# Kernel optimization log

Measured on AMD Instinct MI355X. Metric: run time of the kernel, lower is better.

Reference implementation:

```python
import jax, jax.numpy as jnp
import numpy as np

EPS = 1e-5
NUM_HEADS = 16


def rms_norm(x, w):
    v = jnp.mean(x * x, axis=-1, keepdims=True)
    return x * jax.lax.rsqrt(v + EPS) * w


def rotate_half_interleaved(x):
    # pairs (x0,x1) -> (-x1, x0), interleaved layout
    x1 = x[..., 0::2]
    x2 = x[..., 1::2]
    return jnp.stack([-x2, x1], axis=-1).reshape(x.shape)


def setup_inputs() -> dict:
    key = jax.random.key(0)
    ks = jax.random.split(key, 6)
    B, N, C = 2, 2048, 2048
    D = C // NUM_HEADS
    s = 1.0 / np.sqrt(C)
    return {
        "x": jax.random.normal(ks[0], (B, N, C), jnp.float32),
        "w_qkv": jax.random.normal(ks[1], (3 * C, C), jnp.float32) * s,
        "q_norm_w": jnp.ones((C,), jnp.float32),
        "k_norm_w": jnp.ones((C,), jnp.float32),
        "cos": jnp.cos(jax.random.normal(ks[2], (N, D), jnp.float32)),
        "sin": jnp.sin(jax.random.normal(ks[3], (N, D), jnp.float32)),
        "w_proj": jax.random.normal(ks[4], (C, C), jnp.float32) * s,
        "b_proj": jnp.zeros((C,), jnp.float32),
    }


def reference(x, w_qkv, q_norm_w, k_norm_w, cos, sin, w_proj, b_proj):
    B, N, C = x.shape
    H = NUM_HEADS
    D = C // H
    scale = D ** -0.5

    qkv = jnp.einsum("bnc,fc->bnf", x, w_qkv).reshape(B, N, 3, C)
    q, k, v = qkv[:, :, 0], qkv[:, :, 1], qkv[:, :, 2]

    # RMSNorm over full channel dim C (as in the torch module), then head split
    q = rms_norm(q, q_norm_w).reshape(B, N, H, D)
    k = rms_norm(k, k_norm_w).reshape(B, N, H, D)
    v = v.reshape(B, N, H, D)

    # rotary embedding (head_first=False layout [B,N,H,D])
    c = cos[None, :, None, :]
    s = sin[None, :, None, :]
    q = q * c + rotate_half_interleaved(q) * s
    k = k * c + rotate_half_interleaved(k) * s

    attn = jnp.einsum("bnhd,bmhd->bhnm", q, k) * scale  # [B,H,N,N]
    attn = jax.nn.softmax(attn, axis=-1)
    out = jnp.einsum("bhnm,bmhd->bnhd", attn, v).reshape(B, N, C)
    return jnp.einsum("bnc,oc->bno", out, w_proj) + b_proj
```

## Files before the change

kernel.cpp:

```cpp
#include <hip/hip_runtime.h>
#include <stdint.h>

typedef unsigned short u16;
typedef unsigned int   u32;
typedef _Float16 f16_t;
typedef f16_t f16x8 __attribute__((ext_vector_type(8)));
typedef float  f32x4  __attribute__((ext_vector_type(4)));

#define BB 2
#define NN 2048
#define CC 2048
#define HH 16
#define DD 128
#define FF 6144
#define MM 4096

__device__ __forceinline__ u16 f2h(float f){
    f16_t h = (f16_t)f;
    return __builtin_bit_cast(u16, h);
}
__device__ __forceinline__ float h2f(u16 b){
    return (float)__builtin_bit_cast(f16_t, b);
}
__device__ __forceinline__ f32x4 MFMA(f16x8 a, f16x8 b, f32x4 c){
    return __builtin_amdgcn_mfma_f32_16x16x32_f16(a, b, c, 0, 0, 0);
}
__device__ __forceinline__ void gld16(const void* g, void* l){
    __builtin_amdgcn_global_load_lds(
        (const __attribute__((address_space(1))) void*)(g),
        (__attribute__((address_space(3))) void*)(l), 16, 0, 0);
}
#define SB0() __builtin_amdgcn_sched_barrier(0)

__global__ void k_f2h(const float* __restrict__ a, u16* __restrict__ o, int n4){
    int i = blockIdx.x * blockDim.x + threadIdx.x;
    int stride = gridDim.x * blockDim.x;
    for (; i < n4; i += stride){
        float4 v = ((const float4*)a)[i];
        ushort4 r; r.x = f2h(v.x); r.y = f2h(v.y); r.z = f2h(v.z); r.w = f2h(v.w);
        ((ushort4*)o)[i] = r;
    }
}

template<int OUTH>
__global__ __launch_bounds__(256) void k_gemm_bt(
    const u16* __restrict__ A, const u16* __restrict__ Bw,
    float* __restrict__ outf, u16* __restrict__ outb,
    const float* __restrict__ bias, int M, int N, int K)
{
    __shared__ u16 As[3][128 * 32];
    __shared__ u16 Bs[3][128 * 32];
    const int tid  = threadIdx.x;
    const int brow = blockIdx.y * 128;
    const int bcol = blockIdx.x * 128;
    const int w = tid >> 6, lane = tid & 63;
    const int wr = w >> 1, wc = w & 1;
    const int l15 = lane & 15, g = lane >> 4;
    const int sr  = tid >> 2;
    const int scz = ((tid & 3) ^ ((tid >> 3) & 3)) * 8;
    const int gx  = (g ^ ((l15 >> 1) & 3)) * 8;

    f32x4 acc[4][4];
    #pragma unroll
    for (int i = 0; i < 4; i++)
        #pragma unroll
        for (int j = 0; j < 4; j++){
            f32x4 z = {0.f, 0.f, 0.f, 0.f};
            acc[i][j] = z;
        }

    auto stage = [&](int buf, int k0){
        gld16(&Bw[(size_t)(bcol + sr) * K + k0 + scz],      &Bs[buf][w * 512]);
        gld16(&Bw[(size_t)(bcol + sr + 64) * K + k0 + scz], &Bs[buf][2048 + w * 512]);
        gld16(&A [(size_t)(brow + sr) * K + k0 + scz],      &As[buf][w * 512]);
        gld16(&A [(size_t)(brow + sr + 64) * K + k0 + scz], &As[buf][2048 + w * 512]);
    };

    stage(0, 0);
    stage(1, 32);
    int c = 0;
    for (int k0 = 0; k0 < K; k0 += 32){
        SB0();
        __builtin_amdgcn_s_barrier();
        SB0();
        int ct = c + 2; if (ct >= 3) ct -= 3;
        if (k0 + 64 < K){
            stage(ct, k0 + 64);
            asm volatile("s_waitcnt vmcnt(8)" ::: "memory");
        } else if (k0 + 32 < K){
            asm volatile("s_waitcnt vmcnt(4)" ::: "memory");
        } else {
            asm volatile("s_waitcnt vmcnt(0)" ::: "memory");
        }
        SB0();
        __builtin_amdgcn_s_barrier();
        SB0();
        f16x8 fb[4];
        #pragma unroll
        for (int j = 0; j < 4; j++){
            int row = wc * 64 + j * 16 + l15;
            fb[j] = *(const f16x8*)&Bs[c][row * 32 + gx];
        }
        #pragma unroll
        for (int i = 0; i < 4; i++){
            int row = wr * 64 + i * 16 + l15;
            f16x8 fa = *(const f16x8*)&As[c][row * 32 + gx];
            #pragma unroll
            for (int j = 0; j < 4; j++) acc[i][j] = MFMA(fa, fb[j], acc[i][j]);
        }
        c = (c + 1 == 3) ? 0 : c + 1;
    }

    #pragma unroll
    for (int i = 0; i < 4; i++){
        #pragma unroll
        for (int j = 0; j < 4; j++){
            int colg = bcol + wc * 64 + j * 16 + l15;
            #pragma unroll
            for (int r = 0; r < 4; r++){
                int rowg = brow + wr * 64 + i * 16 + 4 * g + r;
                float v = acc[i][j][r];
                if (OUTH) outb[(size_t)rowg * N + colg] = f2h(v);
                else      outf[(size_t)rowg * N + colg] = v + bias[colg];
            }
        }
    }
}

__global__ __launch_bounds__(256) void k_norm_rope(
    const u16* __restrict__ qkv, const float* __restrict__ qw, const float* __restrict__ kw,
    const float* __restrict__ cosb, const float* __restrict__ sinb,
    u16* __restrict__ qout, u16* __restrict__ kout)
{
    const int m = blockIdx.x;
    const int b = m >> 11;
    const int n = m & 2047;
    const int t = threadIdx.x;
    const size_t base = (size_t)m * FF;
    const int e0 = t * 8;
    const float SCL = 0.08838834764831845f * 1.4426950408889634f;

    float qv[8], kvv[8];
    uint4 qa = *(const uint4*)&qkv[base + e0];
    uint4 ka = *(const uint4*)&qkv[base + CC + e0];
    {
        u32 aa[4] = {qa.x, qa.y, qa.z, qa.w};
        u32 bb[4] = {ka.x, ka.y, ka.z, ka.w};
        #pragma unroll
        for (int i = 0; i < 4; i++){
            qv[2*i]   = h2f((u16)(aa[i] & 0xffff));
            qv[2*i+1] = h2f((u16)(aa[i] >> 16));
            kvv[2*i]   = h2f((u16)(bb[i] & 0xffff));
            kvv[2*i+1] = h2f((u16)(bb[i] >> 16));
        }
    }
    float sq = 0.f, sk = 0.f;
    #pragma unroll
    for (int i = 0; i < 8; i++){ sq += qv[i]*qv[i]; sk += kvv[i]*kvv[i]; }
    #pragma unroll
    for (int o = 32; o > 0; o >>= 1){ sq += __shfl_xor(sq, o); sk += __shfl_xor(sk, o); }
    __shared__ float red[8];
    if ((t & 63) == 0){ red[(t >> 6)*2] = sq; red[(t >> 6)*2 + 1] = sk; }
    __syncthreads();
    sq = red[0] + red[2] + red[4] + red[6];
    sk = red[1] + red[3] + red[5] + red[7];
    const float rq = rsqrtf(sq * (1.f / 2048.f) + 1e-5f);
    const float rk = rsqrtf(sk * (1.f / 2048.f) + 1e-5f);

    const int h  = t >> 4;
    const int d0 = (t & 15) * 8;
    const float* cp = cosb + (size_t)n * DD + d0;
    const float* sp = sinb + (size_t)n * DD + d0;
    float qo[8], ko[8];
    #pragma unroll
    for (int j = 0; j < 8; j += 2){
        float c0 = cp[j], c1 = cp[j+1], s0 = sp[j], s1 = sp[j+1];
        float x0 = qv[j]   * rq * qw[e0 + j];
        float x1 = qv[j+1] * rq * qw[e0 + j + 1];
        qo[j]   = (x0 * c0 - x1 * s0) * SCL;
        qo[j+1] = (x1 * c1 + x0 * s1) * SCL;
        float y0 = kvv[j]   * rk * kw[e0 + j];
        float y1 = kvv[j+1] * rk * kw[e0 + j + 1];
        ko[j]   = y0 * c0 - y1 * s0;
        ko[j+1] = y1 * c1 + y0 * s1;
    }
    const size_t obase = ((size_t)(b * HH + h) * NN + n) * DD + d0;
    uint4 pq, pk;
    pq.x = (u32)f2h(qo[0]) | ((u32)f2h(qo[1]) << 16);
    pq.y = (u32)f2h(qo[2]) | ((u32)f2h(qo[3]) << 16);
    pq.z = (u32)f2h(qo[4]) | ((u32)f2h(qo[5]) << 16);
    pq.w = (u32)f2h(qo[6]) | ((u32)f2h(qo[7]) << 16);
    pk.x = (u32)f2h(ko[0]) | ((u32)f2h(ko[1]) << 16);
    pk.y = (u32)f2h(ko[2]) | ((u32)f2h(ko[3]) << 16);
    pk.z = (u32)f2h(ko[4]) | ((u32)f2h(ko[5]) << 16);
    pk.w = (u32)f2h(ko[6]) | ((u32)f2h(ko[7]) << 16);
    *(uint4*)&qout[obase] = pq;
    *(uint4*)&kout[obase] = pk;
}

__global__ __launch_bounds__(256) void k_vtrans(const u16* __restrict__ qkv, u16* __restrict__ Vt){
    __shared__ u16 t[64 * 66];
    const int bh = blockIdx.z;
    const int b = bh >> 4, h = bh & 15;
    const int n0 = blockIdx.x * 64, d0 = blockIdx.y * 64;
    const int tid = threadIdx.x;
    const int q = tid & 7, p = tid >> 3;
    #pragma unroll
    for (int it = 0; it < 2; it++){
        int r = p + it * 32;
        const u16* src = qkv + (size_t)(b * NN + n0 + r) * FF + 2 * CC + h * DD + d0 + q * 8;
        uint4 v = *(const uint4*)src;
        u32* dst = (u32*)&t[r * 66 + q * 8];
        dst[0] = v.x; dst[1] = v.y; dst[2] = v.z; dst[3] = v.w;
    }
    __syncthreads();
    #pragma unroll
    for (int it = 0; it < 2; it++){
        int rd = p + it * 32;
        u16 o[8];
        #pragma unroll
        for (int j = 0; j < 8; j++) o[j] = t[(q * 8 + j) * 66 + rd];
        *(uint4*)(Vt + ((size_t)bh * DD + d0 + rd) * NN + n0 + q * 8) = *(uint4*)o;
    }
}

__global__ __launch_bounds__(256, 2) void k_attn6(
    const u16* __restrict__ Q, const u16* __restrict__ Kt, const u16* __restrict__ Vt2,
    u16* __restrict__ O)
{
    __shared__ u16 Kbuf[2][8192];
    __shared__ u16 Vbuf[2][8192];
    const int tid = threadIdx.x;
    const int w = tid >> 6, lane = tid & 63;
    const int l15 = lane & 15, g = lane >> 4;
    const int flat = blockIdx.x;
    const int lid  = (flat & 7) * 64 + (flat >> 3);
    const int qb = lid & 15;
    const int h  = (lid >> 4) & 15;
    const int b  = lid >> 8;
    const size_t hb  = (size_t)(b * HH + h) * NN * DD;
    const size_t hbT = (size_t)(b * HH + h) * DD * NN;
    const int qbase = qb * 128 + w * 32;
    const int mperm = 8 * (l15 >> 2) + (l15 & 3);

    f16x8 qf[2][4];
    #pragma unroll
    for (int u = 0; u < 2; u++){
        const u16* qrow = Q + hb + (size_t)(qbase + u * 16 + l15) * DD;
        #pragma unroll
        for (int c = 0; c < 4; c++)
            qf[u][c] = *(const f16x8*)(qrow + c * 32 + 8 * g);
    }

    f32x4 oacc[2][8];
    #pragma unroll
    for (int u = 0; u < 2; u++)
        #pragma unroll
        for (int tb = 0; tb < 8; tb++){ f32x4 z = {0.f,0.f,0.f,0.f}; oacc[u][tb] = z; }
    float lsum0 = 0.f, lsum1 = 0.f;

    auto stage = [&](int buf, int kv0){
        #pragma unroll
        for (int it = 0; it < 8; it++){
            int s = it * 4 + w;
            if (s < 16){
                int hh = s >> 3, t = (s >> 2) & 1, c = s & 3;
                gld16(&Kt[hb + (size_t)(kv0 + 32 * hh + 4 * t + mperm) * DD + 32 * c + 8 * g],
                      &Kbuf[buf][s * 512]);
            } else {
                int s2 = s - 16;
                int hh = s2 >> 3, tb = s2 & 7;
                gld16(&Vt2[hbT + (size_t)(tb * 16 + l15) * NN + kv0 + 32 * hh + 8 * g],
                      &Vbuf[buf][s2 * 512]);
            }
        }
    };

    int cur = 0;
    stage(0, 0);
    for (int kv0 = 0; kv0 < NN; kv0 += 64){
        __syncthreads();
        if (kv0 + 64 < NN) stage(cur ^ 1, kv0 + 64);
        const u16* kb = &Kbuf[cur][0] + lane * 8;
        const u16* vb = &Vbuf[cur][0] + lane * 8;

        f32x4 st[2][4];
        #pragma unroll
        for (int hh = 0; hh < 2; hh++)
            #pragma unroll
            for (int q = 0; q < 4; q++){ f32x4 z = {0.f,0.f,0.f,0.f}; st[hh][q] = z; }
        __builtin_amdgcn_s_setprio(1);
        #pragma unroll
        for (int hh = 0; hh < 2; hh++){
            #pragma unroll
            for (int c = 0; c < 4; c++){
                f16x8 kf0 = *(const f16x8*)(kb + (hh * 8 + c) * 512);
                f16x8 kf1 = *(const f16x8*)(kb + (hh * 8 + 4 + c) * 512);
                st[hh][0] = MFMA(kf0, qf[0][c], st[hh][0]);
                st[hh][1] = MFMA(kf0, qf[1][c], st[hh][1]);
                st[hh][2] = MFMA(kf1, qf[0][c], st[hh][2]);
                st[hh][3] = MFMA(kf1, qf[1][c], st[hh][3]);
            }
        }
        __builtin_amdgcn_s_setprio(0);

        f16x8 pf[2][2];
        #pragma unroll
        for (int hh = 0; hh < 2; hh++){
            #pragma unroll
            for (int r = 0; r < 4; r++){
                float e00 = exp2f(st[hh][0][r]), e10 = exp2f(st[hh][2][r]);
                float e01 = exp2f(st[hh][1][r]), e11 = exp2f(st[hh][3][r]);
                lsum0 += e00 + e10;
                lsum1 += e01 + e11;
                pf[hh][0][r] = (f16_t)e00; pf[hh][0][r + 4] = (f16_t)e10;
                pf[hh][1][r] = (f16_t)e01; pf[hh][1][r + 4] = (f16_t)e11;
            }
        }

        __builtin_amdgcn_s_setprio(1);
        #pragma unroll
        for (int hh = 0; hh < 2; hh++){
            #pragma unroll
            for (int tb = 0; tb < 8; tb++){
                f16x8 vf = *(const f16x8*)(vb + (hh * 8 + tb) * 512);
                oacc[0][tb] = MFMA(pf[hh][0], vf, oacc[0][tb]);
                oacc[1][tb] = MFMA(pf[hh][1], vf, oacc[1][tb]);
            }
        }
        __builtin_amdgcn_s_setprio(0);
        cur ^= 1;
    }

    lsum0 += __shfl_xor(lsum0, 16); lsum0 += __shfl_xor(lsum0, 32);
    lsum1 += __shfl_xor(lsum1, 16); lsum1 += __shfl_xor(lsum1, 32);
    float linv0 = 1.f / lsum0, linv1 = 1.f / lsum1;
    float li0[4], li1[4];
    #pragma unroll
    for (int r = 0; r < 4; r++){
        li0[r] = __shfl(linv0, 4 * g + r);
        li1[r] = __shfl(linv1, 4 * g + r);
    }

    #pragma unroll
    for (int tb = 0; tb < 8; tb++){
        #pragma unroll
        for (int r = 0; r < 4; r++){
            int q0 = qbase + 4 * g + r;
            O[(size_t)(b * NN + q0) * CC + h * DD + tb * 16 + l15] = f2h(oacc[0][tb][r] * li0[r]);
            int q1 = qbase + 16 + 4 * g + r;
            O[(size_t)(b * NN + q1) * CC + h * DD + tb * 16 + l15] = f2h(oacc[1][tb][r] * li1[r]);
        }
    }
}

extern "C" void kernel_launch(void* const* d_in, const int* in_sizes, int n_in,
                              void* d_out, int out_size, void* d_ws, size_t ws_size,
                              hipStream_t stream) {
    const float* x      = (const float*)d_in[0];
    const float* w_qkv  = (const float*)d_in[1];
    const float* qw     = (const float*)d_in[2];
    const float* kw     = (const float*)d_in[3];
    const float* cosb   = (const float*)d_in[4];
    const float* sinb   = (const float*)d_in[5];
    const float* w_proj = (const float*)d_in[6];
    const float* b_proj = (const float*)d_in[7];
    float* out = (float*)d_out;

    const size_t sz_xh   = (size_t)MM * CC * 2;
    const size_t sz_wqkv = (size_t)FF * CC * 2;
    const size_t sz_wprj = (size_t)CC * CC * 2;
    const size_t sz_qkv  = (size_t)MM * FF * 2;
    const size_t sz_t    = (size_t)BB * HH * NN * DD * 2;
    const size_t need = sz_xh + sz_wqkv + sz_wprj + sz_qkv + sz_t*3 + sz_xh;
    if (ws_size < need) return;

    char* ws = (char*)d_ws;
    size_t off = 0;
    auto alloc = [&](size_t bytes){ void* p = ws + off; off += (bytes + 255) & ~(size_t)255; return p; };
    u16* x_h     = (u16*)alloc(sz_xh);
    u16* wqkv_h  = (u16*)alloc(sz_wqkv);
    u16* wprj_h  = (u16*)alloc(sz_wprj);
    u16* qkv     = (u16*)alloc(sz_qkv);
    u16* qr      = (u16*)alloc(sz_t);
    u16* kr      = (u16*)alloc(sz_t);
    u16* vt2     = (u16*)alloc(sz_t);
    u16* ob      = (u16*)alloc(sz_xh);

    k_f2h<<<2048, 256, 0, stream>>>(x, x_h, MM * CC / 4);
    k_f2h<<<2048, 256, 0, stream>>>(w_qkv, wqkv_h, FF * CC / 4);
    k_f2h<<<1024, 256, 0, stream>>>(w_proj, wprj_h, CC * CC / 4);
    k_gemm_bt<1><<<dim3(FF / 128, MM / 128), 256, 0, stream>>>(
        x_h, wqkv_h, nullptr, qkv, nullptr, MM, FF, CC);
    k_norm_rope<<<MM, 256, 0, stream>>>(qkv, qw, kw, cosb, sinb, qr, kr);
    k_vtrans<<<dim3(NN / 64, DD / 64, BB * HH), 256, 0, stream>>>(qkv, vt2);
    k_attn6<<<512, 256, 0, stream>>>(qr, kr, vt2, ob);
    k_gemm_bt<0><<<dim3(CC / 128, MM / 128), 256, 0, stream>>>(
        ob, wprj_h, out, nullptr, b_proj, MM, CC, CC);
}
```

Before: 319.2 us.

## Use 256x256 tile GEMM kernel with 512 threads for QKV projection

Adds a new fp16 MFMA GEMM kernel that computes 256x256 output tiles per block with 8 waves, each wave owning a 128x64 sub-tile, and uses it for the QKV projection. The larger tile raises arithmetic intensity and cuts global/LDS traffic per FLOP compared with the 128x128 kernel. In exchange it uses more registers (32 accumulators per lane) and 96KB of LDS, and launches only 384 blocks, which may lower occupancy and leave the GPU's compute units unevenly loaded.

Measured after the change: 363.9 us. 1.14x slower.

```diff
diff --git a/kernel.cpp b/kernel.cpp
--- a/kernel.cpp
+++ b/kernel.cpp
@@ -39,6 +39,88 @@
         float4 v = ((const float4*)a)[i];
         ushort4 r; r.x = f2h(v.x); r.y = f2h(v.y); r.z = f2h(v.z); r.w = f2h(v.w);
         ((ushort4*)o)[i] = r;
+    }
+}
+
+__global__ __launch_bounds__(512, 2) void k_gemm256(
+    const u16* __restrict__ A, const u16* __restrict__ Bw,
+    u16* __restrict__ outb, int M, int N, int K)
+{
+    __shared__ u16 As[3][256 * 32];
+    __shared__ u16 Bs[3][256 * 32];
+    const int tid  = threadIdx.x;
+    const int brow = blockIdx.y * 256;
+    const int bcol = blockIdx.x * 256;
+    const int w = tid >> 6, lane = tid & 63;
+    const int wr = w >> 2;
+    const int wc = w & 3;
+    const int l15 = lane & 15, g = lane >> 4;
+    const int sr  = tid >> 2;
+    const int scz = ((tid & 3) ^ ((tid >> 3) & 3)) * 8;
+    const int gx  = (g ^ ((l15 >> 1) & 3)) * 8;
+
+    f32x4 acc[8][4];
+    #pragma unroll
+    for (int i = 0; i < 8; i++)
+        #pragma unroll
+        for (int j = 0; j < 4; j++){
+            f32x4 z = {0.f, 0.f, 0.f, 0.f};
+            acc[i][j] = z;
+        }
+
+    auto stage = [&](int buf, int k0){
+        gld16(&A [(size_t)(brow + sr      ) * K + k0 + scz], &As[buf][w * 512]);
+        gld16(&A [(size_t)(brow + sr + 128) * K + k0 + scz], &As[buf][4096 + w * 512]);
+        gld16(&Bw[(size_t)(bcol + sr      ) * K + k0 + scz], &Bs[buf][w * 512]);
+        gld16(&Bw[(size_t)(bcol + sr + 128) * K + k0 + scz], &Bs[buf][4096 + w * 512]);
+    };
+
+    stage(0, 0);
+    stage(1, 32);
+    int c = 0;
+    for (int k0 = 0; k0 < K; k0 += 32){
+        SB0();
+        __builtin_amdgcn_s_barrier();
+        SB0();
+        int ct = c + 2; if (ct >= 3) ct -= 3;
+        if (k0 + 64 < K){
+            stage(ct, k0 + 64);
+            asm volatile("s_waitcnt vmcnt(8)" ::: "memory");
+        } else if (k0 + 32 < K){
+            asm volatile("s_waitcnt vmcnt(4)" ::: "memory");
+        } else {
+            asm volatile("s_waitcnt vmcnt(0)" ::: "memory");
+        }
+        SB0();
+        __builtin_amdgcn_s_barrier();
+        SB0();
+        f16x8 fb[4];
+        #pragma unroll
+        for (int j = 0; j < 4; j++){
+            int row = wc * 64 + j * 16 + l15;
+            fb[j] = *(const f16x8*)&Bs[c][row * 32 + gx];
+        }
+        #pragma unroll
+        for (int i = 0; i < 8; i++){
+            int row = wr * 128 + i * 16 + l15;
+            f16x8 fa = *(const f16x8*)&As[c][row * 32 + gx];
+            #pragma unroll
+            for (int j = 0; j < 4; j++) acc[i][j] = MFMA(fa, fb[j], acc[i][j]);
+        }
+        c = (c + 1 == 3) ? 0 : c + 1;
+    }
+
+    #pragma unroll
+    for (int i = 0; i < 8; i++){
+        #pragma unroll
+        for (int j = 0; j < 4; j++){
+            int colg = bcol + wc * 64 + j * 16 + l15;
+            #pragma unroll
+            for (int r = 0; r < 4; r++){
+                int rowg = brow + wr * 128 + i * 16 + 4 * g + r;
+                outb[(size_t)rowg * N + colg] = f2h(acc[i][j][r]);
+            }
+        }
     }
 }
 
@@ -390,8 +472,8 @@
     k_f2h<<<2048, 256, 0, stream>>>(x, x_h, MM * CC / 4);
     k_f2h<<<2048, 256, 0, stream>>>(w_qkv, wqkv_h, FF * CC / 4);
     k_f2h<<<1024, 256, 0, stream>>>(w_proj, wprj_h, CC * CC / 4);
-    k_gemm_bt<1><<<dim3(FF / 128, MM / 128), 256, 0, stream>>>(
-        x_h, wqkv_h, nullptr, qkv, nullptr, MM, FF, CC);
+    k_gemm256<<<dim3(FF / 256, MM / 256), 512, 0, stream>>>(
+        x_h, wqkv_h, qkv, MM, FF, CC);
     k_norm_rope<<<MM, 256, 0, stream>>>(qkv, qw, kw, cosb, sinb, qr, kr);
     k_vtrans<<<dim3(NN / 64, DD / 64, BB * HH), 256, 0, stream>>>(qkv, vt2);
     k_attn6<<<512, 256, 0, stream>>>(qr, kr, vt2, ob);
```

## Double per-warp query rows in attention and fuse fp16 conversion kernels

Applied to the files above, without the earlier changes.

The attention kernel now gives each warp 64 query rows instead of 32, so each block covers 256 queries and the grid shrinks to 256 blocks. Every K/V tile staged in LDS is therefore reused across twice as many MFMAs, which halves K/V global and LDS traffic per query. The cost is more accumulator registers, launch bounds dropping to one block per SM, and fewer blocks than the MI355X has CUs, so some CUs may sit idle. Separately, the three fp32-to-fp16 conversion launches are merged into one kernel to cut launch overhead.

Result: slower. 339.7 us (+6.4%).

```diff
diff --git a/kernel.cpp b/kernel.cpp
--- a/kernel.cpp
+++ b/kernel.cpp
@@ -32,13 +32,20 @@
 }
 #define SB0() __builtin_amdgcn_sched_barrier(0)
 
-__global__ void k_f2h(const float* __restrict__ a, u16* __restrict__ o, int n4){
+__global__ void k_f2h3(const float* __restrict__ a0, u16* __restrict__ o0, int n0,
+                       const float* __restrict__ a1, u16* __restrict__ o1, int n1,
+                       const float* __restrict__ a2, u16* __restrict__ o2, int n2){
     int i = blockIdx.x * blockDim.x + threadIdx.x;
     int stride = gridDim.x * blockDim.x;
-    for (; i < n4; i += stride){
-        float4 v = ((const float4*)a)[i];
+    int nt = n0 + n1 + n2;
+    for (; i < nt; i += stride){
+        const float4* src; ushort4* dst; int j;
+        if (i < n0){ src = (const float4*)a0; dst = (ushort4*)o0; j = i; }
+        else if (i < n0 + n1){ src = (const float4*)a1; dst = (ushort4*)o1; j = i - n0; }
+        else { src = (const float4*)a2; dst = (ushort4*)o2; j = i - n0 - n1; }
+        float4 v = src[j];
         ushort4 r; r.x = f2h(v.x); r.y = f2h(v.y); r.z = f2h(v.z); r.w = f2h(v.w);
-        ((ushort4*)o)[i] = r;
+        dst[j] = r;
     }
 }
 
@@ -224,7 +231,7 @@
     }
 }
 
-__global__ __launch_bounds__(256, 2) void k_attn6(
+__global__ __launch_bounds__(256, 1) void k_attn7(
     const u16* __restrict__ Q, const u16* __restrict__ Kt, const u16* __restrict__ Vt2,
     u16* __restrict__ O)
 {
@@ -234,30 +241,30 @@
     const int w = tid >> 6, lane = tid & 63;
     const int l15 = lane & 15, g = lane >> 4;
     const int flat = blockIdx.x;
-    const int lid  = (flat & 7) * 64 + (flat >> 3);
-    const int qb = lid & 15;
-    const int h  = (lid >> 4) & 15;
-    const int b  = lid >> 8;
+    const int lid  = (flat & 7) * 32 + (flat >> 3);
+    const int qb = lid & 7;
+    const int h  = (lid >> 3) & 15;
+    const int b  = lid >> 7;
     const size_t hb  = (size_t)(b * HH + h) * NN * DD;
     const size_t hbT = (size_t)(b * HH + h) * DD * NN;
-    const int qbase = qb * 128 + w * 32;
+    const int qbase = qb * 256 + w * 64;
     const int mperm = 8 * (l15 >> 2) + (l15 & 3);
 
-    f16x8 qf[2][4];
-    #pragma unroll
-    for (int u = 0; u < 2; u++){
+    f16x8 qf[4][4];
+    #pragma unroll
+    for (int u = 0; u < 4; u++){
         const u16* qrow = Q + hb + (size_t)(qbase + u * 16 + l15) * DD;
         #pragma unroll
         for (int c = 0; c < 4; c++)
             qf[u][c] = *(const f16x8*)(qrow + c * 32 + 8 * g);
     }
 
-    f32x4 oacc[2][8];
-    #pragma unroll
-    for (int u = 0; u < 2; u++)
+    f32x4 oacc[4][8];
+    #pragma unroll
+    for (int u = 0; u < 4; u++)
         #pragma unroll
         for (int tb = 0; tb < 8; tb++){ f32x4 z = {0.f,0.f,0.f,0.f}; oacc[u][tb] = z; }
-    float lsum0 = 0.f, lsum1 = 0.f;
+    float lsum[4] = {0.f, 0.f, 0.f, 0.f};
 
     auto stage = [&](int buf, int kv0){
         #pragma unroll
@@ -283,73 +290,69 @@
         if (kv0 + 64 < NN) stage(cur ^ 1, kv0 + 64);
         const u16* kb = &Kbuf[cur][0] + lane * 8;
         const u16* vb = &Vbuf[cur][0] + lane * 8;
-
-        f32x4 st[2][4];
-        #pragma unroll
-        for (int hh = 0; hh < 2; hh++)
-            #pragma unroll
-            for (int q = 0; q < 4; q++){ f32x4 z = {0.f,0.f,0.f,0.f}; st[hh][q] = z; }
-        __builtin_amdgcn_s_setprio(1);
         #pragma unroll
         for (int hh = 0; hh < 2; hh++){
+            f32x4 st[4][2];
+            #pragma unroll
+            for (int u = 0; u < 4; u++){
+                f32x4 z = {0.f,0.f,0.f,0.f};
+                st[u][0] = z; st[u][1] = z;
+            }
+            __builtin_amdgcn_s_setprio(1);
             #pragma unroll
             for (int c = 0; c < 4; c++){
                 f16x8 kf0 = *(const f16x8*)(kb + (hh * 8 + c) * 512);
                 f16x8 kf1 = *(const f16x8*)(kb + (hh * 8 + 4 + c) * 512);
-                st[hh][0] = MFMA(kf0, qf[0][c], st[hh][0]);
-                st[hh][1] = MFMA(kf0, qf[1][c], st[hh][1]);
-                st[hh][2] = MFMA(kf1, qf[0][c], st[hh][2]);
-                st[hh][3] = MFMA(kf1, qf[1][c], st[hh][3]);
-            }
-        }
-        __builtin_amdgcn_s_setprio(0);
-
-        f16x8 pf[2][2];
-        #pragma unroll
-        for (int hh = 0; hh < 2; hh++){
-            #pragma unroll
-            for (int r = 0; r < 4; r++){
-                float e00 = exp2f(st[hh][0][r]), e10 = exp2f(st[hh][2][r]);
-                float e01 = exp2f(st[hh][1][r]), e11 = exp2f(st[hh][3][r]);
-                lsum0 += e00 + e10;
-                lsum1 += e01 + e11;
-                pf[hh][0][r] = (f16_t)e00; pf[hh][0][r + 4] = (f16_t)e10;
-                pf[hh][1][r] = (f16_t)e01; pf[hh][1][r + 4] = (f16_t)e11;
-            }
-        }
-
-        __builtin_amdgcn_s_setprio(1);
-        #pragma unroll
-        for (int hh = 0; hh < 2; hh++){
+                #pragma unroll
+                for (int u = 0; u < 4; u++){
+                    st[u][0] = MFMA(kf0, qf[u][c], st[u][0]);
+                    st[u][1] = MFMA(kf1, qf[u][c], st[u][1]);
+                }
+            }
+            __builtin_amdgcn_s_setprio(0);
+            f16x8 pf[4];
+            #pragma unroll
+            for (int u = 0; u < 4; u++){
+                #pragma unroll
+                for (int r = 0; r < 4; r++){
+                    float e0 = exp2f(st[u][0][r]);
+                    float e1 = exp2f(st[u][1][r]);
+                    lsum[u] += e0 + e1;
+                    pf[u][r] = (f16_t)e0; pf[u][r + 4] = (f16_t)e1;
+                }
+            }
+            __builtin_amdgcn_s_setprio(1);
             #pragma unroll
             for (int tb = 0; tb < 8; tb++){
                 f16x8 vf = *(const f16x8*)(vb + (hh * 8 + tb) * 512);
-                oacc[0][tb] = MFMA(pf[hh][0], vf, oacc[0][tb]);
-                oacc[1][tb] = MFMA(pf[hh][1], vf, oacc[1][tb]);
-            }
-        }
-        __builtin_amdgcn_s_setprio(0);
+                #pragma unroll
+                for (int u = 0; u < 4; u++)
+                    oacc[u][tb] = MFMA(pf[u], vf, oacc[u][tb]);
+            }
+            __builtin_amdgcn_s_setprio(0);
+        }
         cur ^= 1;
     }
 
-    lsum0 += __shfl_xor(lsum0, 16); lsum0 += __shfl_xor(lsum0, 32);
-    lsum1 += __shfl_xor(lsum1, 16); lsum1 += __shfl_xor(lsum1, 32);
-    float linv0 = 1.f / lsum0, linv1 = 1.f / lsum1;
-    float li0[4], li1[4];
-    #pragma unroll
-    for (int r = 0; r < 4; r++){
-        li0[r] = __shfl(linv0, 4 * g + r);
-        li1[r] = __shfl(linv1, 4 * g + r);
-    }
-
-    #pragma unroll
-    for (int tb = 0; tb < 8; tb++){
-        #pragma unroll
-        for (int r = 0; r < 4; r++){
-            int q0 = qbase + 4 * g + r;
-            O[(size_t)(b * NN + q0) * CC + h * DD + tb * 16 + l15] = f2h(oacc[0][tb][r] * li0[r]);
-            int q1 = qbase + 16 + 4 * g + r;
-            O[(size_t)(b * NN + q1) * CC + h * DD + tb * 16 + l15] = f2h(oacc[1][tb][r] * li1[r]);
+    float li[4][4];
+    #pragma unroll
+    for (int u = 0; u < 4; u++){
+        lsum[u] += __shfl_xor(lsum[u], 16);
+        lsum[u] += __shfl_xor(lsum[u], 32);
+        float linv = 1.f / lsum[u];
+        #pragma unroll
+        for (int r = 0; r < 4; r++) li[u][r] = __shfl(linv, 4 * g + r);
+    }
+
+    #pragma unroll
+    for (int u = 0; u < 4; u++){
+        #pragma unroll
+        for (int tb = 0; tb < 8; tb++){
+            #pragma unroll
+            for (int r = 0; r < 4; r++){
+                int q0 = qbase + u * 16 + 4 * g + r;
+                O[(size_t)(b * NN + q0) * CC + h * DD + tb * 16 + l15] = f2h(oacc[u][tb][r] * li[u][r]);
+            }
         }
     }
 }
@@ -387,14 +390,14 @@
     u16* vt2     = (u16*)alloc(sz_t);
     u16* ob      = (u16*)alloc(sz_xh);
 
-    k_f2h<<<2048, 256, 0, stream>>>(x, x_h, MM * CC / 4);
-    k_f2h<<<2048, 256, 0, stream>>>(w_qkv, wqkv_h, FF * CC / 4);
-    k_f2h<<<1024, 256, 0, stream>>>(w_proj, wprj_h, CC * CC / 4);
+    k_f2h3<<<2048, 256, 0, stream>>>(x, x_h, MM * CC / 4,
+                                     w_qkv, wqkv_h, FF * CC / 4,
+                                     w_proj, wprj_h, CC * CC / 4);
     k_gemm_bt<1><<<dim3(FF / 128, MM / 128), 256, 0, stream>>>(
         x_h, wqkv_h, nullptr, qkv, nullptr, MM, FF, CC);
     k_norm_rope<<<MM, 256, 0, stream>>>(qkv, qw, kw, cosb, sinb, qr, kr);
     k_vtrans<<<dim3(NN / 64, DD / 64, BB * HH), 256, 0, stream>>>(qkv, vt2);
-    k_attn6<<<512, 256, 0, stream>>>(qr, kr, vt2, ob);
+    k_attn7<<<256, 256, 0, stream>>>(qr, kr, vt2, ob);
     k_gemm_bt<0><<<dim3(CC / 128, MM / 128), 256, 0, stream>>>(
         ob, wprj_h, out, nullptr, b_proj, MM, CC, CC);
 }
```
